# Performance work log

Measured on AMD Instinct MI355X. Metric: run time of the kernel, lower is better.

The kernel has to match this reference:

```python
import jax, jax.numpy as jnp
import numpy as np

N_R, N_U, N_P = 40000, 30000, 30000
N = N_R + N_U + N_P
E = 1600000
NFEAT, NHID, NCLASS = 128, 128, 40


def setup_inputs() -> dict:
    key = jax.random.key(0)
    ks = jax.random.split(key, 12)
    s = 0.05
    return {
        "inputx_r": jax.random.normal(ks[0], (N_R, 5), jnp.float32),
        "inputx_u": jax.random.normal(ks[1], (N_U, 7), jnp.float32),
        "inputx_p": jax.random.normal(ks[2], (N_P, 6), jnp.float32),
        "edge_index": jax.random.randint(ks[3], (2, E), 0, N, jnp.int64)
            if jax.config.jax_enable_x64 else jax.random.randint(ks[3], (2, E), 0, N, jnp.int32),
        "W_r": jax.random.normal(ks[4], (5, NFEAT), jnp.float32) * s,
        "b_r": jax.random.normal(ks[5], (NFEAT,), jnp.float32) * s,
        "W_u": jax.random.normal(ks[6], (7, NFEAT), jnp.float32) * s,
        "b_u": jax.random.normal(ks[7], (NFEAT,), jnp.float32) * s,
        "W_p": jax.random.normal(ks[8], (6, NFEAT), jnp.float32) * s,
        "b_p": jax.random.normal(ks[9], (NFEAT,), jnp.float32) * s,
        "W1": jax.random.normal(ks[10], (NFEAT, NHID), jnp.float32) * s,
        "W2": jax.random.normal(ks[11], (NHID, NCLASS), jnp.float32) * s,
    }


def _gcn_conv(x, W, src, dst, num_nodes):
    # GCNConv(add_self_loops=False, normalize=False, bias=False):
    # out = A @ (x @ W), unit edge weights, aggregation at dst of source messages.
    h = x @ W                                      # [N, d_out]
    return jax.ops.segment_sum(h[src], dst, num_segments=num_nodes)


def reference(inputx_r, inputx_u, inputx_p, edge_index,
              W_r, b_r, W_u, b_u, W_p, b_p, W1, W2):
    # Segment-wise input projections (nums = [[N_R, N_R+N_U], [.,.], [.,.]]
    # with empty 2nd/3rd blocks; tail is the p-segment), then two GCN layers.
    x = jnp.concatenate([
        inputx_r @ W_r + b_r,   # nodes [0 : N_R]
        inputx_u @ W_u + b_u,   # nodes [N_R : N_R+N_U]
        inputx_p @ W_p + b_p,   # nodes [N_R+N_U : N]
    ], axis=0)                  # [N, NFEAT]
    src, dst = edge_index[0], edge_index[1]
    h = jax.nn.relu(_gcn_conv(x, W1, src, dst, N))   # gc1 + relu
    # dropout: inference (training=False) -> identity
    out = _gcn_conv(h, W2, src, dst, N)              # gc2
    return out
```

## Files before the change

### kernel.cpp

```cpp
#include <hip/hip_runtime.h>

constexpr int kNR = 40000;
constexpr int kNU = 30000;
constexpr int kNP = 30000;
constexpr int kN  = 100000;
constexpr int kE  = 1600000;
constexpr int kF  = 128;
constexpr int kC  = 40;
constexpr int kBN = 64;
constexpr int kNB = (kN + kBN - 1) / kBN;
constexpr int kNBp = 1600;
constexpr int kSlot = 2048;
constexpr int kPackB = 98;
constexpr int kFuseB = kPackB;
constexpr int kW2B   = kPackB + 1;
constexpr int kScat0 = kPackB + 2;
constexpr int kScatB = 128;
constexpr int kCE    = kE / kScatB;
constexpr int kPrepB = kScat0 + kScatB;

typedef __attribute__((ext_vector_type(8))) short bf16x8;
typedef __attribute__((ext_vector_type(4))) float f32x4;

__device__ __forceinline__ float bf_to_f(unsigned short h) {
    union { unsigned int i; float f; } u; u.i = ((unsigned int)h) << 16; return u.f;
}
__device__ __forceinline__ unsigned short f_to_bf(float f) {
    union { unsigned int i; float f; } u; u.f = f;
    unsigned int r = u.i + 0x7FFFu + ((u.i >> 16) & 1u);
    return (unsigned short)(r >> 16);
}
__device__ __forceinline__ float2 bf2_to_f2(unsigned int p) {
    union { unsigned int i; float f; } lo, hi;
    lo.i = (p & 0xFFFFu) << 16;
    hi.i = p & 0xFFFF0000u;
    return make_float2(lo.f, hi.f);
}
__device__ __forceinline__ unsigned int pack_bf2(float a, float b) {
    return (unsigned int)f_to_bf(a) | ((unsigned int)f_to_bf(b) << 16);
}
__device__ __forceinline__ float ldf(const void* p, int i, int isbf) {
    return isbf ? bf_to_f(((const unsigned short*)p)[i]) : ((const float*)p)[i];
}
__device__ __forceinline__ int lde(const int* p, int i, int is64) {
    return is64 ? p[2 * i] : p[i];
}

__device__ __forceinline__ int sniff_isbf(const void* W1, int t, int* sh) {
    if (t < 64) {
        unsigned int wv = ((const unsigned int*)W1)[t];
        unsigned int ax = wv & 0x7FFFu;
        int pl = (ax == 0u) || (ax > 0x2000u && ax < 0x4000u);
        unsigned long long mk = __ballot(pl);
        if (t == 0) *sh = (__popcll(mk) >= 48) ? 1 : 0;
    }
    __syncthreads();
    return *sh;
}

__global__ void __launch_bounds__(1024) gcn_prep(
        const void* __restrict__ xr, const void* __restrict__ xu, const void* __restrict__ xp,
        const void* __restrict__ Wr, const void* __restrict__ br,
        const void* __restrict__ Wu, const void* __restrict__ bu,
        const void* __restrict__ Wp, const void* __restrict__ bp,
        const void* __restrict__ W1, const void* __restrict__ W2,
        const int* __restrict__ ei,
        unsigned short* __restrict__ fwfrag, unsigned short* __restrict__ w2frag,
        uint4* __restrict__ xpack, int* __restrict__ gcnt,
        unsigned int* __restrict__ slots) {
    __shared__ __align__(16) char smem[29696];
    __shared__ int sflag;
    int t = threadIdx.x;
    int bx = blockIdx.x;
    if (bx < kPackB) {
        int isbf = sniff_isbf(W1, t, &sflag);
        int n = bx * 1024 + t;
        if (n >= kN) return;
        const void* base; int roff, d;
        if (n < kNR)            { base = xr; roff = n * 5;               d = 5; }
        else if (n < kNR + kNU) { base = xu; roff = (n - kNR) * 7;       d = 7; }
        else                    { base = xp; roff = (n - kNR - kNU) * 6; d = 6; }
        float f[8];
        #pragma unroll
        for (int i = 0; i < 8; i++) f[i] = (i < d) ? ldf(base, roff + i, isbf) : 0.f;
        uint4 u;
        u.x = pack_bf2(f[0], f[1]);  u.y = pack_bf2(f[2], f[3]);
        u.z = pack_bf2(f[4], f[5]);  u.w = pack_bf2(f[6], f[7]);
        xpack[n] = u;
    } else if (bx == kFuseB) {
        int isbf = sniff_isbf(W1, t, &sflag);
        float* sw   = (float*)smem;
        float* pacc = (float*)(smem + 10752);
        unsigned short* flds = (unsigned short*)(smem + 21504);
        for (int i = t; i < 21 * kF; i += 1024) {
            int r = i >> 7, c = i & 127;
            float v;
            if (r < 5)        v = ldf(Wr, r * kF + c, isbf);
            else if (r < 12)  v = ldf(Wu, (r - 5) * kF + c, isbf);
            else if (r < 18)  v = ldf(Wp, (r - 12) * kF + c, isbf);
            else if (r == 18) v = ldf(br, c, isbf);
            else if (r == 19) v = ldf(bu, c, isbf);
            else              v = ldf(bp, c, isbf);
            sw[i] = v;
        }
        __syncthreads();
        {
            bool active = (t < 256);
            int j = t & 127, half = (t >> 7) & 1;
            float acc[21];
            #pragma unroll
            for (int r = 0; r < 21; r++) acc[r] = 0.f;
            if (active) {
                int k0 = half * 64, k1 = k0 + 64;
                for (int k = k0; k < k1; k++) {
                    float w1 = ldf(W1, k * kF + j, isbf);
                    #pragma unroll
                    for (int r = 0; r < 21; r++) acc[r] += sw[r * kF + k] * w1;
                }
            }
            if (active && half == 1) {
                #pragma unroll
                for (int r = 0; r < 21; r++) pacc[r * kF + j] = acc[r];
            }
            __syncthreads();
            if (active && half == 0) {
                #pragma unroll
                for (int r = 0; r < 21; r++) acc[r] += pacc[r * kF + j];
                unsigned short row[32];
                #pragma unroll
                for (int s = 0; s < 32; s++) row[s] = 0;
                #pragma unroll
                for (int i = 0; i < 5; i++) row[0  + i] = f_to_bf(acc[i]);
                #pragma unroll
                for (int i = 0; i < 7; i++) row[8  + i] = f_to_bf(acc[5 + i]);
                #pragma unroll
                for (int i = 0; i < 6; i++) row[16 + i] = f_to_bf(acc[12 + i]);
                row[24] = f_to_bf(acc[18]);  row[25] = f_to_bf(acc[19]);  row[26] = f_to_bf(acc[20]);
                #pragma unroll
                for (int s = 0; s < 32; s++) flds[j * 32 + s] = row[s];
            }
        }
        __syncthreads();
        for (int idx = t; idx < 8 * 64; idx += 1024) {
            int t8 = idx >> 6, lane = idx & 63;
            int mm = lane & 15, q = lane >> 4;
            #pragma unroll
            for (int j = 0; j < 8; j++)
                fwfrag[idx * 8 + j] = flds[(16 * t8 + mm) * 32 + q * 8 + j];
        }
    } else if (bx == kW2B) {
        int isbf = sniff_isbf(W1, t, &sflag);
        for (int idx = t; idx < 12 * 64; idx += 1024) {
            int st = idx >> 6, lane = idx & 63;
            int s = st / 3, tt = st % 3;
            int mm = lane & 15, q = lane >> 4;
            int cls = 16 * tt + mm;
            #pragma unroll
            for (int j = 0; j < 8; j++) {
                int k = s * 32 + q * 8 + j;
                w2frag[idx * 8 + j] = (cls < kC) ? f_to_bf(ldf(W2, k * kC + cls, isbf))
                                                 : (unsigned short)0;
            }
        }
    } else {
        int* hist = (int*)smem;
        int* cur  = (int*)(smem + 6400);
        if (t < 64) {
            int v = ((const int*)ei)[2 * t + 1];
            unsigned long long mk = __ballot(v != 0);
            if (t == 0) sflag = (mk == 0ull) ? 1 : 0;
        }
        for (int i = t; i < kNBp; i += 1024) hist[i] = 0;
        __syncthreads();
        int is64 = sflag;
        int blk = bx - kScat0;
        int e0 = blk * kCE, e1 = e0 + kCE;
        for (int eb = e0 + t; eb < e1; eb += 4096) {
            unsigned int d[4];
            #pragma unroll
            for (int j = 0; j < 4; j++) {
                int e = eb + j * 1024;
                d[j] = (e < e1) ? (unsigned int)lde(ei, kE + e, is64) : 0xFFFFFFFFu;
            }
            #pragma unroll
            for (int j = 0; j < 4; j++)
                if (d[j] < (unsigned int)kN) atomicAdd(&hist[d[j] >> 6], 1);
        }
        __syncthreads();
        int off = (blk * 401) % kNBp;
        for (int j = t; j < kNBp; j += 1024) {
            int i = j + off;
            if (i >= kNBp) i -= kNBp;
            int h = hist[i];
            cur[i] = (h > 0) ? atomicAdd(&gcnt[i], h) : 0;
        }
        __syncthreads();
        for (int eb = e0 + t; eb < e1; eb += 4096) {
            unsigned int d[4], s[4];
            #pragma unroll
            for (int j = 0; j < 4; j++) {
                int e = eb + j * 1024;
                d[j] = (e < e1) ? (unsigned int)lde(ei, kE + e, is64) : 0xFFFFFFFFu;
            }
            #pragma unroll
            for (int j = 0; j < 4; j++) {
                int e = eb + j * 1024;
                s[j] = (e < e1) ? (unsigned int)lde(ei, e, is64) : 0u;
            }
            #pragma unroll
            for (int j = 0; j < 4; j++) {
                if (d[j] < (unsigned int)kN) {
                    unsigned int sv = (s[j] < (unsigned int)kN) ? s[j] : 0u;
                    int b = (int)(d[j] >> 6);
                    int pos = atomicAdd(&cur[b], 1);
                    if (pos < kSlot) slots[(size_t)b * kSlot + pos] = (sv << 6) | (d[j] & 63u);
                }
            }
        }
    }
}

__global__ void __launch_bounds__(256) GCN_2190433321521_kernel(
        const unsigned int* __restrict__ slots,
        const int* __restrict__ gcnt,
        const uint4* __restrict__ xpack,
        const unsigned short* __restrict__ fwfrag,
        const unsigned short* __restrict__ w2frag,
        int* __restrict__ rpb,
        int* __restrict__ rpe,
        int* __restrict__ col,
        unsigned short* __restrict__ hw) {
    __shared__ __align__(16) char smem[25600];
    float*          agg_l  = (float*)smem;
    int*            cnt_l  = (int*)(smem + 7424);
    int*            strt_l = (int*)(smem + 7680);
    int*            cntv_l = (int*)(smem + 7936);
    unsigned int*   wst    = (unsigned int*)(smem + 8192);
    int*            col_l  = (int*)(smem + 16384);
    unsigned short* hbuf   = (unsigned short*)(smem + 8192);
    unsigned short* cst    = (unsigned short*)smem;

    int b = blockIdx.x;
    int base = b * kBN;
    int nn = min(kBN, kN - base);
    int tid = threadIdx.x;

    if (tid < kBN) cnt_l[tid] = 0;
    __syncthreads();
    int p0 = b * kSlot;
    int m = min(gcnt[b], kSlot);
    int p1 = p0 + m;

    for (int ib = p0 + tid; ib < p1; ib += 1024) {
        unsigned int w[4]; int ok[4];
        #pragma unroll
        for (int j = 0; j < 4; j++) {
            int i = ib + j * 256;
            ok[j] = (i < p1);
            w[j] = ok[j] ? slots[i] : 0u;
        }
        #pragma unroll
        for (int j = 0; j < 4; j++) {
            int i = ib + j * 256;
            if (ok[j]) {
                wst[i - p0] = w[j];
                atomicAdd(&cnt_l[w[j] & 63u], 1);
            }
        }
    }
    __syncthreads();
    if (tid < 64) {
        int v = cnt_l[tid];
        int incl = v;
        #pragma unroll
        for (int o = 1; o < 64; o <<= 1) {
            int y = __shfl_up(incl, o, 64);
            if (tid >= o) incl += y;
        }
        int cursor = p0 + incl - v;
        cnt_l[tid]  = cursor;
        strt_l[tid] = cursor;
        cntv_l[tid] = v;
        if (tid < nn) { rpb[base + tid] = cursor; rpe[base + tid] = cursor + v; }
    }
    __syncthreads();

    for (int i = p0 + tid; i < p1; i += 256) {
        unsigned int w = wst[i - p0];
        unsigned int s = w >> 6;
        int dloc = (int)(w & 63u);
        int pos = atomicAdd(&cnt_l[dloc], 1);
        col_l[pos - p0] = (int)s;
    }
    __syncthreads();
    for (int i = tid; i < m; i += 256) col[p0 + i] = col_l[i];

    {
        int node = tid >> 2, j = tid & 3;
        float aR[8], aU[8], aP[8];
        #pragma unroll
        for (int i = 0; i < 8; i++) { aR[i] = 0.f; aU[i] = 0.f; aP[i] = 0.f; }
        float cR = 0.f, cU = 0.f, cP = 0.f;
        int start = strt_l[node] - p0;
        int c = cntv_l[node];
        for (int i = start + j; i < start + c; i += 4) {
            int s = col_l[i];
            uint4 u = xpack[s];
            float2 q0 = bf2_to_f2(u.x), q1 = bf2_to_f2(u.y);
            float2 q2 = bf2_to_f2(u.z), q3 = bf2_to_f2(u.w);
            if (s < kNR) {
                aR[0]+=q0.x; aR[1]+=q0.y; aR[2]+=q1.x; aR[3]+=q1.y;
                aR[4]+=q2.x; aR[5]+=q2.y; aR[6]+=q3.x; aR[7]+=q3.y; cR += 1.f;
            } else if (s < kNR + kNU) {
                aU[0]+=q0.x; aU[1]+=q0.y; aU[2]+=q1.x; aU[3]+=q1.y;
                aU[4]+=q2.x; aU[5]+=q2.y; aU[6]+=q3.x; aU[7]+=q3.y; cU += 1.f;
            } else {
                aP[0]+=q0.x; aP[1]+=q0.y; aP[2]+=q1.x; aP[3]+=q1.y;
                aP[4]+=q2.x; aP[5]+=q2.y; aP[6]+=q3.x; aP[7]+=q3.y; cP += 1.f;
            }
        }
        #pragma unroll
        for (int i = 0; i < 8; i++) {
            float v = aR[i];
            v += __shfl_xor(v, 1, 64);  v += __shfl_xor(v, 2, 64);
            if (j == 0) agg_l[node * 29 + i] = v;
        }
        #pragma unroll
        for (int i = 0; i < 8; i++) {
            float v = aU[i];
            v += __shfl_xor(v, 1, 64);  v += __shfl_xor(v, 2, 64);
            if (j == 0) agg_l[node * 29 + 8 + i] = v;
        }
        #pragma unroll
        for (int i = 0; i < 8; i++) {
            float v = aP[i];
            v += __shfl_xor(v, 1, 64);  v += __shfl_xor(v, 2, 64);
            if (j == 0) agg_l[node * 29 + 16 + i] = v;
        }
        float v = cR;
        v += __shfl_xor(v, 1, 64);  v += __shfl_xor(v, 2, 64);
        if (j == 0) agg_l[node * 29 + 24] = v;
        v = cU;
        v += __shfl_xor(v, 1, 64);  v += __shfl_xor(v, 2, 64);
        if (j == 0) agg_l[node * 29 + 25] = v;
        v = cP;
        v += __shfl_xor(v, 1, 64);  v += __shfl_xor(v, 2, 64);
        if (j == 0) agg_l[node * 29 + 26] = v;
    }
    __syncthreads();

    int wid = tid >> 6, lane = tid & 63;
    int mm = lane & 15, q = lane >> 4;
    int node = wid * 16 + mm;
    bf16x8 a1;
    #pragma unroll
    for (int j = 0; j < 8; j++) {
        int sl = q * 8 + j;
        a1[j] = (sl < 27) ? (short)f_to_bf(agg_l[node * 29 + sl]) : (short)0;
    }
    __syncthreads();
    const bf16x8* fwf = (const bf16x8*)fwfrag;
    f32x4 c1[8];
    #pragma unroll
    for (int t = 0; t < 8; t++) {
        f32x4 z = {0.f, 0.f, 0.f, 0.f};
        c1[t] = __builtin_amdgcn_mfma_f32_16x16x32_bf16(a1, fwf[t * 64 + lane], z, 0, 0, 0);
    }
    unsigned short* hb = hbuf + wid * 16 * 136;
    #pragma unroll
    for (int t = 0; t < 8; t++) {
        #pragma unroll
        for (int r = 0; r < 4; r++)
            hb[(q * 4 + r) * 136 + 16 * t + mm] = f_to_bf(fmaxf(c1[t][r], 0.f));
    }
    const bf16x8* w2f = (const bf16x8*)w2frag;
    f32x4 c2[3];
    #pragma unroll
    for (int t = 0; t < 3; t++) { c2[t].x = 0.f; c2[t].y = 0.f; c2[t].z = 0.f; c2[t].w = 0.f; }
    #pragma unroll
    for (int s = 0; s < 4; s++) {
        bf16x8 a2 = *(const bf16x8*)&hb[mm * 136 + s * 32 + q * 8];
        #pragma unroll
        for (int t = 0; t < 3; t++)
            c2[t] = __builtin_amdgcn_mfma_f32_16x16x32_bf16(a2, w2f[(s * 3 + t) * 64 + lane],
                                                            c2[t], 0, 0, 0);
    }
    #pragma unroll
    for (int t = 0; t < 3; t++) {
        int cls = 16 * t + mm;
        if (cls < kC) {
            #pragma unroll
            for (int r = 0; r < 4; r++)
                cst[(wid * 16 + q * 4 + r) * kC + cls] = f_to_bf(c2[t][r]);
        }
    }
    __syncthreads();
    {
        int tot = nn * (kC / 2);
        const unsigned int* cs32 = (const unsigned int*)cst;
        unsigned int* ho = (unsigned int*)(hw + (size_t)base * kC);
        for (int i = tid; i < tot; i += 256) ho[i] = cs32[i];
    }
}

__global__ void __launch_bounds__(256) gcn_gather2(const unsigned int* __restrict__ hw32,
                                                   const int* __restrict__ rpb,
                                                   const int* __restrict__ rpe,
                                                   const int* __restrict__ col,
                                                   unsigned int* __restrict__ out,
                                                   const void* __restrict__ W1) {
    __shared__ int sisbf;
    int t = threadIdx.x;
    int isbf = sniff_isbf(W1, t, &sisbf);
    int w = (blockIdx.x * 256 + t) >> 6;
    if (w >= kN) return;
    int lane = t & 63;
    int grp = lane / 10;
    int cp  = lane % 10;
    int beg = rpb[w], end = rpe[w];
    float f0 = 0.f, f1 = 0.f, f2 = 0.f, f3 = 0.f;
    if (grp < 6) {
        const uint2* hp = (const uint2*)hw32;
        int e = beg + grp;
        int c0 = (e      < end) ? col[e]      : -1;
        int c1 = (e + 6  < end) ? col[e + 6]  : -1;
        int c2 = (e + 12 < end) ? col[e + 12] : -1;
        int c3 = (e + 18 < end) ? col[e + 18] : -1;
        if (c0 >= 0) {
            uint2 v = hp[c0 * 10 + cp];
            float2 a = bf2_to_f2(v.x), bb = bf2_to_f2(v.y);
            f0 += a.x; f1 += a.y; f2 += bb.x; f3 += bb.y;
        }
        if (c1 >= 0) {
            uint2 v = hp[c1 * 10 + cp];
            float2 a = bf2_to_f2(v.x), bb = bf2_to_f2(v.y);
            f0 += a.x; f1 += a.y; f2 += bb.x; f3 += bb.y;
        }
        if (c2 >= 0) {
            uint2 v = hp[c2 * 10 + cp];
            float2 a = bf2_to_f2(v.x), bb = bf2_to_f2(v.y);
            f0 += a.x; f1 += a.y; f2 += bb.x; f3 += bb.y;
        }
        if (c3 >= 0) {
            uint2 v = hp[c3 * 10 + cp];
            float2 a = bf2_to_f2(v.x), bb = bf2_to_f2(v.y);
            f0 += a.x; f1 += a.y; f2 += bb.x; f3 += bb.y;
        }
        for (e += 24; e < end; e += 6) {
            int s = col[e];
            uint2 v = hp[s * 10 + cp];
            float2 a = bf2_to_f2(v.x), bb = bf2_to_f2(v.y);
            f0 += a.x; f1 += a.y; f2 += bb.x; f3 += bb.y;
        }
    }
    f0 += __shfl(f0, lane + 30, 64);
    f1 += __shfl(f1, lane + 30, 64);
    f2 += __shfl(f2, lane + 30, 64);
    f3 += __shfl(f3, lane + 30, 64);
    f0 += __shfl(f0, lane + 10, 64) + __shfl(f0, lane + 20, 64);
    f1 += __shfl(f1, lane + 10, 64) + __shfl(f1, lane + 20, 64);
    f2 += __shfl(f2, lane + 10, 64) + __shfl(f2, lane + 20, 64);
    f3 += __shfl(f3, lane + 10, 64) + __shfl(f3, lane + 20, 64);
    if (lane < 10) {
        if (isbf) {
            out[w * 20 + 2 * lane]     = pack_bf2(f0, f1);
            out[w * 20 + 2 * lane + 1] = pack_bf2(f2, f3);
        } else {
            float* of = (float*)out;
            of[w * 40 + 4 * lane]     = f0;
            of[w * 40 + 4 * lane + 1] = f1;
            of[w * 40 + 4 * lane + 2] = f2;
            of[w * 40 + 4 * lane + 3] = f3;
        }
    }
}

extern "C" void kernel_launch(void* const* d_in, const int* in_sizes, int n_in,
                              void* d_out, int out_size, void* d_ws, size_t ws_size,
                              hipStream_t stream) {
    const void* xr = d_in[0];
    const void* xu = d_in[1];
    const void* xp = d_in[2];
    const int*  ei = (const int*)d_in[3];
    const void* Wr = d_in[4];
    const void* br = d_in[5];
    const void* Wu = d_in[6];
    const void* bu = d_in[7];
    const void* Wp = d_in[8];
    const void* bp = d_in[9];
    const void* W1 = d_in[10];
    const void* W2 = d_in[11];
    (void)in_sizes; (void)n_in; (void)out_size; (void)ws_size;

    char* ws = (char*)d_ws;
    size_t off = 0;
    auto alloc = [&](size_t bytes) -> void* {
        void* p = (void*)(ws + off);
        off = (off + bytes + 255) & ~(size_t)255;
        return p;
    };
    int*            gcnt   = (int*)           alloc((size_t)kNBp * 4);
    unsigned short* fwfrag = (unsigned short*)alloc(8 * 64 * 8 * 2);
    unsigned short* w2frag = (unsigned short*)alloc(12 * 64 * 8 * 2);
    uint4*          xpack  = (uint4*)         alloc((size_t)kN * 16);
    unsigned int*   slots  = (unsigned int*)  alloc((size_t)kNB * kSlot * 4);
    int*            col    = (int*)           alloc((size_t)kNB * kSlot * 4);
    int*            rpb    = (int*)           alloc((size_t)kN * 4);
    int*            rpe    = (int*)           alloc((size_t)kN * 4);
    unsigned short* hwb    = (unsigned short*)alloc((size_t)kN * kC * 2);

    hipMemsetAsync(gcnt, 0, (size_t)kNBp * 4, stream);
    gcn_prep<<<kPrepB, 1024, 0, stream>>>(xr, xu, xp, Wr, br, Wu, bu, Wp, bp, W1, W2,
                                          ei, fwfrag, w2frag, xpack, gcnt, slots);
    GCN_2190433321521_kernel<<<kNB, 256, 0, stream>>>(slots, gcnt, xpack, fwfrag, w2frag,
                                                      rpb, rpe, col, hwb);
    gcn_gather2<<<(kN * 64 + 255) / 256, 256, 0, stream>>>((const unsigned int*)hwb, rpb, rpe,
                                                           col, (unsigned int*)d_out, W1);
}
```

Measured before the change: 176.7 us.

## Widen gather loads, prefetch neighbor rows, and register-cache edges in scatter

The scatter prep doubles its block count and loads each block's edges into registers once, reusing them for both the histogram and the slot-writing passes instead of reading the edge list twice. The layer-1 aggregation loop software-prefetches the next neighbor's packed row while the current one is accumulated. The second-layer gather now uses 16-byte loads with 12 edge groups of 5 lanes per node instead of 8-byte loads with 6 groups of 10, and writes its output as wide vector stores. These changes target memory latency and load count on the irregular gathers, at the cost of more registers per thread and a deeper shuffle reduction.

Result: slower. 188.1 us (+6.5%).

```diff
diff --git a/kernel.cpp b/kernel.cpp
--- a/kernel.cpp
+++ b/kernel.cpp
@@ -15,8 +15,9 @@
 constexpr int kFuseB = kPackB;
 constexpr int kW2B   = kPackB + 1;
 constexpr int kScat0 = kPackB + 2;
-constexpr int kScatB = 128;
+constexpr int kScatB = 256;
 constexpr int kCE    = kE / kScatB;
+constexpr int kEPT   = (kCE + 1023) / 1024;
 constexpr int kPrepB = kScat0 + kScatB;
 
 typedef __attribute__((ext_vector_type(8))) short bf16x8;
@@ -175,17 +176,17 @@
         int is64 = sflag;
         int blk = bx - kScat0;
         int e0 = blk * kCE, e1 = e0 + kCE;
-        for (int eb = e0 + t; eb < e1; eb += 4096) {
-            unsigned int d[4];
-            #pragma unroll
-            for (int j = 0; j < 4; j++) {
-                int e = eb + j * 1024;
-                d[j] = (e < e1) ? (unsigned int)lde(ei, kE + e, is64) : 0xFFFFFFFFu;
-            }
-            #pragma unroll
-            for (int j = 0; j < 4; j++)
-                if (d[j] < (unsigned int)kN) atomicAdd(&hist[d[j] >> 6], 1);
-        }
+        unsigned int dv[kEPT], sv[kEPT];
+        #pragma unroll
+        for (int it = 0; it < kEPT; it++) {
+            int e = e0 + t + it * 1024;
+            bool ok = (e < e1);
+            dv[it] = ok ? (unsigned int)lde(ei, kE + e, is64) : 0xFFFFFFFFu;
+            sv[it] = ok ? (unsigned int)lde(ei, e, is64) : 0u;
+        }
+        #pragma unroll
+        for (int it = 0; it < kEPT; it++)
+            if (dv[it] < (unsigned int)kN) atomicAdd(&hist[dv[it] >> 6], 1);
         __syncthreads();
         int off = (blk * 401) % kNBp;
         for (int j = t; j < kNBp; j += 1024) {
@@ -195,26 +196,13 @@
             cur[i] = (h > 0) ? atomicAdd(&gcnt[i], h) : 0;
         }
         __syncthreads();
-        for (int eb = e0 + t; eb < e1; eb += 4096) {
-            unsigned int d[4], s[4];
-            #pragma unroll
-            for (int j = 0; j < 4; j++) {
-                int e = eb + j * 1024;
-                d[j] = (e < e1) ? (unsigned int)lde(ei, kE + e, is64) : 0xFFFFFFFFu;
-            }
-            #pragma unroll
-            for (int j = 0; j < 4; j++) {
-                int e = eb + j * 1024;
-                s[j] = (e < e1) ? (unsigned int)lde(ei, e, is64) : 0u;
-            }
-            #pragma unroll
-            for (int j = 0; j < 4; j++) {
-                if (d[j] < (unsigned int)kN) {
-                    unsigned int sv = (s[j] < (unsigned int)kN) ? s[j] : 0u;
-                    int b = (int)(d[j] >> 6);
-                    int pos = atomicAdd(&cur[b], 1);
-                    if (pos < kSlot) slots[(size_t)b * kSlot + pos] = (sv << 6) | (d[j] & 63u);
-                }
+        #pragma unroll
+        for (int it = 0; it < kEPT; it++) {
+            if (dv[it] < (unsigned int)kN) {
+                unsigned int sval = (sv[it] < (unsigned int)kN) ? sv[it] : 0u;
+                int b = (int)(dv[it] >> 6);
+                int pos = atomicAdd(&cur[b], 1);
+                if (pos < kSlot) slots[(size_t)b * kSlot + pos] = (sval << 6) | (dv[it] & 63u);
             }
         }
     }
@@ -302,10 +290,16 @@
         for (int i = 0; i < 8; i++) { aR[i] = 0.f; aU[i] = 0.f; aP[i] = 0.f; }
         float cR = 0.f, cU = 0.f, cP = 0.f;
         int start = strt_l[node] - p0;
-        int c = cntv_l[node];
-        for (int i = start + j; i < start + c; i += 4) {
-            int s = col_l[i];
-            uint4 u = xpack[s];
+        int iend = start + cntv_l[node];
+        int i = start + j;
+        int sN = (i < iend) ? col_l[i] : -1;
+        uint4 uN = make_uint4(0u, 0u, 0u, 0u);
+        if (sN >= 0) uN = xpack[sN];
+        while (sN >= 0) {
+            int s = sN; uint4 u = uN;
+            i += 4;
+            sN = (i < iend) ? col_l[i] : -1;
+            if (sN >= 0) uN = xpack[sN];
             float2 q0 = bf2_to_f2(u.x), q1 = bf2_to_f2(u.y);
             float2 q2 = bf2_to_f2(u.z), q3 = bf2_to_f2(u.w);
             if (s < kNR) {
@@ -320,22 +314,22 @@
             }
         }
         #pragma unroll
-        for (int i = 0; i < 8; i++) {
-            float v = aR[i];
+        for (int i2 = 0; i2 < 8; i2++) {
+            float v = aR[i2];
             v += __shfl_xor(v, 1, 64);  v += __shfl_xor(v, 2, 64);
-            if (j == 0) agg_l[node * 29 + i] = v;
-        }
-        #pragma unroll
-        for (int i = 0; i < 8; i++) {
-            float v = aU[i];
+            if (j == 0) agg_l[node * 29 + i2] = v;
+        }
+        #pragma unroll
+        for (int i2 = 0; i2 < 8; i2++) {
+            float v = aU[i2];
             v += __shfl_xor(v, 1, 64);  v += __shfl_xor(v, 2, 64);
-            if (j == 0) agg_l[node * 29 + 8 + i] = v;
-        }
-        #pragma unroll
-        for (int i = 0; i < 8; i++) {
-            float v = aP[i];
+            if (j == 0) agg_l[node * 29 + 8 + i2] = v;
+        }
+        #pragma unroll
+        for (int i2 = 0; i2 < 8; i2++) {
+            float v = aP[i2];
             v += __shfl_xor(v, 1, 64);  v += __shfl_xor(v, 2, 64);
-            if (j == 0) agg_l[node * 29 + 16 + i] = v;
+            if (j == 0) agg_l[node * 29 + 16 + i2] = v;
         }
         float v = cR;
         v += __shfl_xor(v, 1, 64);  v += __shfl_xor(v, 2, 64);
@@ -415,62 +409,51 @@
     int w = (blockIdx.x * 256 + t) >> 6;
     if (w >= kN) return;
     int lane = t & 63;
-    int grp = lane / 10;
-    int cp  = lane % 10;
+    int grp = lane / 5;
+    int cp  = lane % 5;
     int beg = rpb[w], end = rpe[w];
-    float f0 = 0.f, f1 = 0.f, f2 = 0.f, f3 = 0.f;
-    if (grp < 6) {
-        const uint2* hp = (const uint2*)hw32;
+    float f0 = 0.f, f1 = 0.f, f2 = 0.f, f3 = 0.f, f4 = 0.f, f5 = 0.f, f6 = 0.f, f7 = 0.f;
+    if (grp < 12) {
+        const uint4* hp = (const uint4*)hw32;
+        auto acc = [&](uint4 u) {
+            float2 a0 = bf2_to_f2(u.x), a1 = bf2_to_f2(u.y);
+            float2 a2 = bf2_to_f2(u.z), a3 = bf2_to_f2(u.w);
+            f0 += a0.x; f1 += a0.y; f2 += a1.x; f3 += a1.y;
+            f4 += a2.x; f5 += a2.y; f6 += a3.x; f7 += a3.y;
+        };
         int e = beg + grp;
         int c0 = (e      < end) ? col[e]      : -1;
-        int c1 = (e + 6  < end) ? col[e + 6]  : -1;
-        int c2 = (e + 12 < end) ? col[e + 12] : -1;
-        int c3 = (e + 18 < end) ? col[e + 18] : -1;
-        if (c0 >= 0) {
-            uint2 v = hp[c0 * 10 + cp];
-            float2 a = bf2_to_f2(v.x), bb = bf2_to_f2(v.y);
-            f0 += a.x; f1 += a.y; f2 += bb.x; f3 += bb.y;
-        }
-        if (c1 >= 0) {
-            uint2 v = hp[c1 * 10 + cp];
-            float2 a = bf2_to_f2(v.x), bb = bf2_to_f2(v.y);
-            f0 += a.x; f1 += a.y; f2 += bb.x; f3 += bb.y;
-        }
-        if (c2 >= 0) {
-            uint2 v = hp[c2 * 10 + cp];
-            float2 a = bf2_to_f2(v.x), bb = bf2_to_f2(v.y);
-            f0 += a.x; f1 += a.y; f2 += bb.x; f3 += bb.y;
-        }
-        if (c3 >= 0) {
-            uint2 v = hp[c3 * 10 + cp];
-            float2 a = bf2_to_f2(v.x), bb = bf2_to_f2(v.y);
-            f0 += a.x; f1 += a.y; f2 += bb.x; f3 += bb.y;
-        }
-        for (e += 24; e < end; e += 6) {
-            int s = col[e];
-            uint2 v = hp[s * 10 + cp];
-            float2 a = bf2_to_f2(v.x), bb = bf2_to_f2(v.y);
-            f0 += a.x; f1 += a.y; f2 += bb.x; f3 += bb.y;
-        }
-    }
-    f0 += __shfl(f0, lane + 30, 64);
-    f1 += __shfl(f1, lane + 30, 64);
-    f2 += __shfl(f2, lane + 30, 64);
-    f3 += __shfl(f3, lane + 30, 64);
-    f0 += __shfl(f0, lane + 10, 64) + __shfl(f0, lane + 20, 64);
-    f1 += __shfl(f1, lane + 10, 64) + __shfl(f1, lane + 20, 64);
-    f2 += __shfl(f2, lane + 10, 64) + __shfl(f2, lane + 20, 64);
-    f3 += __shfl(f3, lane + 10, 64) + __shfl(f3, lane + 20, 64);
-    if (lane < 10) {
+        int c1 = (e + 12 < end) ? col[e + 12] : -1;
+        if (c0 >= 0) acc(hp[(size_t)c0 * 5 + cp]);
+        if (c1 >= 0) acc(hp[(size_t)c1 * 5 + cp]);
+        for (e += 24; e < end; e += 12) acc(hp[(size_t)col[e] * 5 + cp]);
+    }
+    f0 += __shfl(f0, lane + 30, 64);  f1 += __shfl(f1, lane + 30, 64);
+    f2 += __shfl(f2, lane + 30, 64);  f3 += __shfl(f3, lane + 30, 64);
+    f4 += __shfl(f4, lane + 30, 64);  f5 += __shfl(f5, lane + 30, 64);
+    f6 += __shfl(f6, lane + 30, 64);  f7 += __shfl(f7, lane + 30, 64);
+    f0 += __shfl(f0, lane + 15, 64);  f1 += __shfl(f1, lane + 15, 64);
+    f2 += __shfl(f2, lane + 15, 64);  f3 += __shfl(f3, lane + 15, 64);
+    f4 += __shfl(f4, lane + 15, 64);  f5 += __shfl(f5, lane + 15, 64);
+    f6 += __shfl(f6, lane + 15, 64);  f7 += __shfl(f7, lane + 15, 64);
+    f0 += __shfl(f0, lane + 5, 64) + __shfl(f0, lane + 10, 64);
+    f1 += __shfl(f1, lane + 5, 64) + __shfl(f1, lane + 10, 64);
+    f2 += __shfl(f2, lane + 5, 64) + __shfl(f2, lane + 10, 64);
+    f3 += __shfl(f3, lane + 5, 64) + __shfl(f3, lane + 10, 64);
+    f4 += __shfl(f4, lane + 5, 64) + __shfl(f4, lane + 10, 64);
+    f5 += __shfl(f5, lane + 5, 64) + __shfl(f5, lane + 10, 64);
+    f6 += __shfl(f6, lane + 5, 64) + __shfl(f6, lane + 10, 64);
+    f7 += __shfl(f7, lane + 5, 64) + __shfl(f7, lane + 10, 64);
+    if (lane < 5) {
         if (isbf) {
-            out[w * 20 + 2 * lane]     = pack_bf2(f0, f1);
-            out[w * 20 + 2 * lane + 1] = pack_bf2(f2, f3);
+            uint4 o;
+            o.x = pack_bf2(f0, f1);  o.y = pack_bf2(f2, f3);
+            o.z = pack_bf2(f4, f5);  o.w = pack_bf2(f6, f7);
+            ((uint4*)out)[(size_t)w * 5 + lane] = o;
         } else {
-            float* of = (float*)out;
-            of[w * 40 + 4 * lane]     = f0;
-            of[w * 40 + 4 * lane + 1] = f1;
-            of[w * 40 + 4 * lane + 2] = f2;
-            of[w * 40 + 4 * lane + 3] = f3;
+            float4* of = (float4*)out;
+            of[(size_t)w * 10 + 2 * lane]     = make_float4(f0, f1, f2, f3);
+            of[(size_t)w * 10 + 2 * lane + 1] = make_float4(f4, f5, f6, f7);
         }
     }
 }
```

## Widen scatter and fused-layer parallelism, keep edges in registers, swizzle gather blocks

Applied to the files above, without the earlier changes.

The scatter stage now uses twice as many blocks. Each thread loads its src/dst edges into registers once and reuses them for both the histogram and the slot-scatter pass, so the edge_index is no longer read twice. The fused GCN kernel goes from 256 to 512 threads, with 8 lanes per node in the aggregation loop; only the first four waves run the MFMA stages. The second gather remaps block IDs in groups of 8, which looks aimed at spreading work across XCDs for cache locality. The risks are higher register pressure in the scatter, idle waves during the MFMA stage, and more contention on the global gcnt atomics.

New measurement: 186.4 us. 1.06x slower.

```diff
diff --git a/kernel.cpp b/kernel.cpp
--- a/kernel.cpp
+++ b/kernel.cpp
@@ -15,9 +15,12 @@
 constexpr int kFuseB = kPackB;
 constexpr int kW2B   = kPackB + 1;
 constexpr int kScat0 = kPackB + 2;
-constexpr int kScatB = 128;
+constexpr int kScatB = 256;
 constexpr int kCE    = kE / kScatB;
+constexpr int kEPT   = (kCE + 1023) / 1024;
 constexpr int kPrepB = kScat0 + kScatB;
+constexpr int kGB2 = (kN * 64) / 256;
+constexpr int kGQ  = kGB2 / 8;
 
 typedef __attribute__((ext_vector_type(8))) short bf16x8;
 typedef __attribute__((ext_vector_type(4))) float f32x4;
@@ -175,17 +178,17 @@
         int is64 = sflag;
         int blk = bx - kScat0;
         int e0 = blk * kCE, e1 = e0 + kCE;
-        for (int eb = e0 + t; eb < e1; eb += 4096) {
-            unsigned int d[4];
-            #pragma unroll
-            for (int j = 0; j < 4; j++) {
-                int e = eb + j * 1024;
-                d[j] = (e < e1) ? (unsigned int)lde(ei, kE + e, is64) : 0xFFFFFFFFu;
-            }
-            #pragma unroll
-            for (int j = 0; j < 4; j++)
-                if (d[j] < (unsigned int)kN) atomicAdd(&hist[d[j] >> 6], 1);
-        }
+        unsigned int dv[kEPT], sv[kEPT];
+        #pragma unroll
+        for (int it = 0; it < kEPT; it++) {
+            int e = e0 + t + it * 1024;
+            bool ok = (e < e1);
+            dv[it] = ok ? (unsigned int)lde(ei, kE + e, is64) : 0xFFFFFFFFu;
+            sv[it] = ok ? (unsigned int)lde(ei, e, is64) : 0u;
+        }
+        #pragma unroll
+        for (int it = 0; it < kEPT; it++)
+            if (dv[it] < (unsigned int)kN) atomicAdd(&hist[dv[it] >> 6], 1);
         __syncthreads();
         int off = (blk * 401) % kNBp;
         for (int j = t; j < kNBp; j += 1024) {
@@ -195,32 +198,19 @@
             cur[i] = (h > 0) ? atomicAdd(&gcnt[i], h) : 0;
         }
         __syncthreads();
-        for (int eb = e0 + t; eb < e1; eb += 4096) {
-            unsigned int d[4], s[4];
-            #pragma unroll
-            for (int j = 0; j < 4; j++) {
-                int e = eb + j * 1024;
-                d[j] = (e < e1) ? (unsigned int)lde(ei, kE + e, is64) : 0xFFFFFFFFu;
-            }
-            #pragma unroll
-            for (int j = 0; j < 4; j++) {
-                int e = eb + j * 1024;
-                s[j] = (e < e1) ? (unsigned int)lde(ei, e, is64) : 0u;
-            }
-            #pragma unroll
-            for (int j = 0; j < 4; j++) {
-                if (d[j] < (unsigned int)kN) {
-                    unsigned int sv = (s[j] < (unsigned int)kN) ? s[j] : 0u;
-                    int b = (int)(d[j] >> 6);
-                    int pos = atomicAdd(&cur[b], 1);
-                    if (pos < kSlot) slots[(size_t)b * kSlot + pos] = (sv << 6) | (d[j] & 63u);
-                }
-            }
-        }
-    }
-}
-
-__global__ void __launch_bounds__(256) GCN_2190433321521_kernel(
+        #pragma unroll
+        for (int it = 0; it < kEPT; it++) {
+            if (dv[it] < (unsigned int)kN) {
+                unsigned int sval = (sv[it] < (unsigned int)kN) ? sv[it] : 0u;
+                int b = (int)(dv[it] >> 6);
+                int pos = atomicAdd(&cur[b], 1);
+                if (pos < kSlot) slots[(size_t)b * kSlot + pos] = (sval << 6) | (dv[it] & 63u);
+            }
+        }
+    }
+}
+
+__global__ void __launch_bounds__(512) GCN_2190433321521_kernel(
         const unsigned int* __restrict__ slots,
         const int* __restrict__ gcnt,
         const uint4* __restrict__ xpack,
@@ -251,17 +241,17 @@
     int m = min(gcnt[b], kSlot);
     int p1 = p0 + m;
 
-    for (int ib = p0 + tid; ib < p1; ib += 1024) {
+    for (int ib = p0 + tid; ib < p1; ib += 2048) {
         unsigned int w[4]; int ok[4];
         #pragma unroll
         for (int j = 0; j < 4; j++) {
-            int i = ib + j * 256;
+            int i = ib + j * 512;
             ok[j] = (i < p1);
             w[j] = ok[j] ? slots[i] : 0u;
         }
         #pragma unroll
         for (int j = 0; j < 4; j++) {
-            int i = ib + j * 256;
+            int i = ib + j * 512;
             if (ok[j]) {
                 wst[i - p0] = w[j];
                 atomicAdd(&cnt_l[w[j] & 63u], 1);
@@ -285,7 +275,7 @@
     }
     __syncthreads();
 
-    for (int i = p0 + tid; i < p1; i += 256) {
+    for (int i = p0 + tid; i < p1; i += 512) {
         unsigned int w = wst[i - p0];
         unsigned int s = w >> 6;
         int dloc = (int)(w & 63u);
@@ -293,17 +283,17 @@
         col_l[pos - p0] = (int)s;
     }
     __syncthreads();
-    for (int i = tid; i < m; i += 256) col[p0 + i] = col_l[i];
+    for (int i = tid; i < m; i += 512) col[p0 + i] = col_l[i];
 
     {
-        int node = tid >> 2, j = tid & 3;
+        int node = tid >> 3, j = tid & 7;
         float aR[8], aU[8], aP[8];
         #pragma unroll
         for (int i = 0; i < 8; i++) { aR[i] = 0.f; aU[i] = 0.f; aP[i] = 0.f; }
         float cR = 0.f, cU = 0.f, cP = 0.f;
         int start = strt_l[node] - p0;
         int c = cntv_l[node];
-        for (int i = start + j; i < start + c; i += 4) {
+        for (int i = start + j; i < start + c; i += 8) {
             int s = col_l[i];
             uint4 u = xpack[s];
             float2 q0 = bf2_to_f2(u.x), q1 = bf2_to_f2(u.y);
@@ -320,78 +310,82 @@
             }
         }
         #pragma unroll
-        for (int i = 0; i < 8; i++) {
-            float v = aR[i];
-            v += __shfl_xor(v, 1, 64);  v += __shfl_xor(v, 2, 64);
-            if (j == 0) agg_l[node * 29 + i] = v;
-        }
-        #pragma unroll
-        for (int i = 0; i < 8; i++) {
-            float v = aU[i];
-            v += __shfl_xor(v, 1, 64);  v += __shfl_xor(v, 2, 64);
-            if (j == 0) agg_l[node * 29 + 8 + i] = v;
-        }
-        #pragma unroll
-        for (int i = 0; i < 8; i++) {
-            float v = aP[i];
-            v += __shfl_xor(v, 1, 64);  v += __shfl_xor(v, 2, 64);
-            if (j == 0) agg_l[node * 29 + 16 + i] = v;
+        for (int i2 = 0; i2 < 8; i2++) {
+            float v = aR[i2];
+            v += __shfl_xor(v, 1, 64);  v += __shfl_xor(v, 2, 64);  v += __shfl_xor(v, 4, 64);
+            if (j == 0) agg_l[node * 29 + i2] = v;
+        }
+        #pragma unroll
+        for (int i2 = 0; i2 < 8; i2++) {
+            float v = aU[i2];
+            v += __shfl_xor(v, 1, 64);  v += __shfl_xor(v, 2, 64);  v += __shfl_xor(v, 4, 64);
+            if (j == 0) agg_l[node * 29 + 8 + i2] = v;
+        }
+        #pragma unroll
+        for (int i2 = 0; i2 < 8; i2++) {
+            float v = aP[i2];
+            v += __shfl_xor(v, 1, 64);  v += __shfl_xor(v, 2, 64);  v += __shfl_xor(v, 4, 64);
+            if (j == 0) agg_l[node * 29 + 16 + i2] = v;
         }
         float v = cR;
-        v += __shfl_xor(v, 1, 64);  v += __shfl_xor(v, 2, 64);
+        v += __shfl_xor(v, 1, 64);  v += __shfl_xor(v, 2, 64);  v += __shfl_xor(v, 4, 64);
         if (j == 0) agg_l[node * 29 + 24] = v;
         v = cU;
-        v += __shfl_xor(v, 1, 64);  v += __shfl_xor(v, 2, 64);
+        v += __shfl_xor(v, 1, 64);  v += __shfl_xor(v, 2, 64);  v += __shfl_xor(v, 4, 64);
         if (j == 0) agg_l[node * 29 + 25] = v;
         v = cP;
-        v += __shfl_xor(v, 1, 64);  v += __shfl_xor(v, 2, 64);
+        v += __shfl_xor(v, 1, 64);  v += __shfl_xor(v, 2, 64);  v += __shfl_xor(v, 4, 64);
         if (j == 0) agg_l[node * 29 + 26] = v;
     }
     __syncthreads();
 
     int wid = tid >> 6, lane = tid & 63;
     int mm = lane & 15, q = lane >> 4;
-    int node = wid * 16 + mm;
     bf16x8 a1;
-    #pragma unroll
-    for (int j = 0; j < 8; j++) {
-        int sl = q * 8 + j;
-        a1[j] = (sl < 27) ? (short)f_to_bf(agg_l[node * 29 + sl]) : (short)0;
-    }
-    __syncthreads();
-    const bf16x8* fwf = (const bf16x8*)fwfrag;
-    f32x4 c1[8];
-    #pragma unroll
-    for (int t = 0; t < 8; t++) {
-        f32x4 z = {0.f, 0.f, 0.f, 0.f};
-        c1[t] = __builtin_amdgcn_mfma_f32_16x16x32_bf16(a1, fwf[t * 64 + lane], z, 0, 0, 0);
-    }
-    unsigned short* hb = hbuf + wid * 16 * 136;
-    #pragma unroll
-    for (int t = 0; t < 8; t++) {
-        #pragma unroll
-        for (int r = 0; r < 4; r++)
-            hb[(q * 4 + r) * 136 + 16 * t + mm] = f_to_bf(fmaxf(c1[t][r], 0.f));
-    }
-    const bf16x8* w2f = (const bf16x8*)w2frag;
-    f32x4 c2[3];
-    #pragma unroll
-    for (int t = 0; t < 3; t++) { c2[t].x = 0.f; c2[t].y = 0.f; c2[t].z = 0.f; c2[t].w = 0.f; }
-    #pragma unroll
-    for (int s = 0; s < 4; s++) {
-        bf16x8 a2 = *(const bf16x8*)&hb[mm * 136 + s * 32 + q * 8];
-        #pragma unroll
-        for (int t = 0; t < 3; t++)
-            c2[t] = __builtin_amdgcn_mfma_f32_16x16x32_bf16(a2, w2f[(s * 3 + t) * 64 + lane],
-                                                            c2[t], 0, 0, 0);
-    }
-    #pragma unroll
-    for (int t = 0; t < 3; t++) {
-        int cls = 16 * t + mm;
-        if (cls < kC) {
+    if (wid < 4) {
+        int node = wid * 16 + mm;
+        #pragma unroll
+        for (int j = 0; j < 8; j++) {
+            int sl = q * 8 + j;
+            a1[j] = (sl < 27) ? (short)f_to_bf(agg_l[node * 29 + sl]) : (short)0;
+        }
+    }
+    __syncthreads();
+    if (wid < 4) {
+        const bf16x8* fwf = (const bf16x8*)fwfrag;
+        f32x4 c1[8];
+        #pragma unroll
+        for (int t = 0; t < 8; t++) {
+            f32x4 z = {0.f, 0.f, 0.f, 0.f};
+            c1[t] = __builtin_amdgcn_mfma_f32_16x16x32_bf16(a1, fwf[t * 64 + lane], z, 0, 0, 0);
+        }
+        unsigned short* hb = hbuf + wid * 16 * 136;
+        #pragma unroll
+        for (int t = 0; t < 8; t++) {
             #pragma unroll
             for (int r = 0; r < 4; r++)
-                cst[(wid * 16 + q * 4 + r) * kC + cls] = f_to_bf(c2[t][r]);
+                hb[(q * 4 + r) * 136 + 16 * t + mm] = f_to_bf(fmaxf(c1[t][r], 0.f));
+        }
+        const bf16x8* w2f = (const bf16x8*)w2frag;
+        f32x4 c2[3];
+        #pragma unroll
+        for (int t = 0; t < 3; t++) { c2[t].x = 0.f; c2[t].y = 0.f; c2[t].z = 0.f; c2[t].w = 0.f; }
+        #pragma unroll
+        for (int s = 0; s < 4; s++) {
+            bf16x8 a2 = *(const bf16x8*)&hb[mm * 136 + s * 32 + q * 8];
+            #pragma unroll
+            for (int t = 0; t < 3; t++)
+                c2[t] = __builtin_amdgcn_mfma_f32_16x16x32_bf16(a2, w2f[(s * 3 + t) * 64 + lane],
+                                                                c2[t], 0, 0, 0);
+        }
+        #pragma unroll
+        for (int t = 0; t < 3; t++) {
+            int cls = 16 * t + mm;
+            if (cls < kC) {
+                #pragma unroll
+                for (int r = 0; r < 4; r++)
+                    cst[(wid * 16 + q * 4 + r) * kC + cls] = f_to_bf(c2[t][r]);
+            }
         }
     }
     __syncthreads();
@@ -399,7 +393,7 @@
         int tot = nn * (kC / 2);
         const unsigned int* cs32 = (const unsigned int*)cst;
         unsigned int* ho = (unsigned int*)(hw + (size_t)base * kC);
-        for (int i = tid; i < tot; i += 256) ho[i] = cs32[i];
+        for (int i = tid; i < tot; i += 512) ho[i] = cs32[i];
     }
 }
 
@@ -412,7 +406,9 @@
     __shared__ int sisbf;
     int t = threadIdx.x;
     int isbf = sniff_isbf(W1, t, &sisbf);
-    int w = (blockIdx.x * 256 + t) >> 6;
+    int bid = blockIdx.x;
+    int swb = (bid & 7) * kGQ + (bid >> 3);
+    int w = swb * 4 + (t >> 6);
     if (w >= kN) return;
     int lane = t & 63;
     int grp = lane / 10;
@@ -512,8 +508,8 @@
     hipMemsetAsync(gcnt, 0, (size_t)kNBp * 4, stream);
     gcn_prep<<<kPrepB, 1024, 0, stream>>>(xr, xu, xp, Wr, br, Wu, bu, Wp, bp, W1, W2,
                                           ei, fwfrag, w2frag, xpack, gcnt, slots);
-    GCN_2190433321521_kernel<<<kNB, 256, 0, stream>>>(slots, gcnt, xpack, fwfrag, w2frag,
+    GCN_2190433321521_kernel<<<kNB, 512, 0, stream>>>(slots, gcnt, xpack, fwfrag, w2frag,
                                                       rpb, rpe, col, hwb);
-    gcn_gather2<<<(kN * 64 + 255) / 256, 256, 0, stream>>>((const unsigned int*)hwb, rpb, rpe,
-                                                           col, (unsigned int*)d_out, W1);
-}
+    gcn_gather2<<<kGB2, 256, 0, stream>>>((const unsigned int*)hwb, rpb, rpe,
+                                          col, (unsigned int*)d_out, W1);
+}
```
